# Performance work log

Measured on AMD Instinct MI355X. Metric: run time of the kernel, lower is better.

Reference implementation:

```python
import jax, jax.numpy as jnp
import numpy as np

B, T, I, H, C = 4096, 512, 3, 32, 3  # batch, seq_len, input, hidden, classes


def setup_inputs() -> dict:
    key = jax.random.key(0)
    ks = jax.random.split(key, 7)
    s = 1.0 / np.sqrt(H)  # PyTorch LSTM init scale
    return {
        "x": jax.random.normal(ks[0], (B, T, I), dtype=jnp.float32),
        "W_ih": jax.random.normal(ks[1], (4 * H, I), dtype=jnp.float32) * s,
        "W_hh": jax.random.normal(ks[2], (4 * H, H), dtype=jnp.float32) * s,
        "b_ih": jax.random.normal(ks[3], (4 * H,), dtype=jnp.float32) * s,
        "b_hh": jax.random.normal(ks[4], (4 * H,), dtype=jnp.float32) * s,
        "W_fc": jax.random.normal(ks[5], (C, H), dtype=jnp.float32) * s,
        "b_fc": jax.random.normal(ks[6], (C,), dtype=jnp.float32) * s,
    }


def reference(x, W_ih, W_hh, b_ih, b_hh, W_fc, b_fc):
    # Precompute input contribution to all gates for every timestep: (B,T,4H)
    xg = jnp.einsum("bti,gi->btg", x, W_ih) + b_ih + b_hh
    h0 = jnp.zeros((x.shape[0], H), dtype=x.dtype)
    c0 = jnp.zeros_like(h0)

    def step(carry, xt):
        h, c = carry
        g = xt + h @ W_hh.T  # (B,4H)
        i_g, f_g, g_g, o_g = jnp.split(g, 4, axis=-1)  # PyTorch gate order i,f,g,o
        i_g = jax.nn.sigmoid(i_g)
        f_g = jax.nn.sigmoid(f_g)
        g_g = jnp.tanh(g_g)
        o_g = jax.nn.sigmoid(o_g)
        c = f_g * c + i_g * g_g
        h = o_g * jnp.tanh(c)
        return (h, c), None

    (h_last, _), _ = jax.lax.scan(step, (h0, c0), jnp.swapaxes(xg, 0, 1))
    return h_last @ W_fc.T + b_fc  # (B, num_classes)
```

## Files before the change

kernel.cpp:

```cpp
#include <hip/hip_runtime.h>
#include <cstdint>

#define B_TOT 4096
#define T_LEN 512
#define CHUNK 128
#define LOG2E 1.44269504088896340736f
#define HSTR  40

typedef _Float16 f16x8 __attribute__((ext_vector_type(8)));
typedef _Float16 f16x4 __attribute__((ext_vector_type(4)));
typedef float    f32x4 __attribute__((ext_vector_type(4)));

__device__ __forceinline__ float ex2(float v)  { return __builtin_amdgcn_exp2f(v); }
__device__ __forceinline__ float rcp_(float v) { return __builtin_amdgcn_rcpf(v); }

__global__ __launch_bounds__(256, 2)
void lstm_b8p(const float* __restrict__ x,
              const float* __restrict__ W_ih,
              const float* __restrict__ W_hh,
              const float* __restrict__ b_ih,
              const float* __restrict__ b_hh,
              const float* __restrict__ W_fc,
              const float* __restrict__ b_fc,
              float* __restrict__ out)
{
    __shared__ __align__(16) _Float16 hbuf[2][8][HSTR];
    __shared__ __align__(16) _Float16 xbuf[CHUNK][8][4];

    const int tid  = threadIdx.x;
    const int wave = tid >> 6;
    const int lane = tid & 63;
    const int n    = lane & 15;
    const int kq   = lane >> 4;
    const int nb   = n & 7;
    const int tb   = blockIdx.x * 8;

    const int   gate_m = n & 3;
    const int   hl_m   = n >> 2;
    const int   R1     = gate_m * 32 + 8 * wave + hl_m;
    const int   R2     = R1 + 4;
    const float sm     = (gate_m == 2) ? (-2.0f * LOG2E) : (-LOG2E);

    f16x8 aW1, aW2;
#pragma unroll
    for (int j = 0; j < 8; ++j) {
        aW1[j] = (_Float16)(sm * W_hh[R1 * 32 + 8 * kq + j]);
        aW2[j] = (_Float16)(sm * W_hh[R2 * 32 + 8 * kq + j]);
    }
    f16x8 a21 = {}, a22 = {};
    if (kq == 0) {
        a21[0] = (_Float16)(sm * W_ih[R1 * 3 + 0]);
        a21[1] = (_Float16)(sm * W_ih[R1 * 3 + 1]);
        a21[2] = (_Float16)(sm * W_ih[R1 * 3 + 2]);
        a21[3] = (_Float16)(sm * (b_ih[R1] + b_hh[R1]));
        a22[0] = (_Float16)(sm * W_ih[R2 * 3 + 0]);
        a22[1] = (_Float16)(sm * W_ih[R2 * 3 + 1]);
        a22[2] = (_Float16)(sm * W_ih[R2 * 3 + 2]);
        a22[3] = (_Float16)(sm * (b_ih[R2] + b_hh[R2]));
    }

    const int hid_s = 8 * wave + kq + ((n >> 3) ? 4 : 0);

    if (tid < 160) ((int*)&hbuf[0][0][0])[tid] = 0;

    const float K2 = -2.0f * LOG2E;
    float c = 0.0f;
    const f32x4 z = {0.f, 0.f, 0.f, 0.f};
    f32x4 accx1, accx2;

    if (blockIdx.x & 256) __builtin_amdgcn_s_sleep(5);

    for (int tc = 0; tc < T_LEN; tc += CHUNK) {
#pragma unroll
        for (int s = 0; s < 4; ++s) {
            const int idx = tid + s * 256;
            const int tl = idx >> 3, m = idx & 7;
            const float* xp = x + ((size_t)(tb + m) * T_LEN + (tc + tl)) * 3;
            f16x4 v;
            v[0] = (_Float16)xp[0]; v[1] = (_Float16)xp[1];
            v[2] = (_Float16)xp[2]; v[3] = (_Float16)1.0f;
            *(f16x4*)&xbuf[tl][m][0] = v;
        }
        __syncthreads();

        {
            const f16x4 xv = *(const f16x4*)&xbuf[0][nb][0];
            const f16x8 b2 = __builtin_shufflevector(xv, xv, 0, 1, 2, 3, 0, 1, 2, 3);
            accx1 = __builtin_amdgcn_mfma_f32_16x16x32_f16(a21, b2, z, 0, 0, 0);
            accx2 = __builtin_amdgcn_mfma_f32_16x16x32_f16(a22, b2, z, 0, 0, 0);
        }

#pragma unroll 2
        for (int tt = 0; tt < CHUNK; ++tt) {
            const int p = tt & 1;

            const f16x8 bh  = *(const f16x8*)&hbuf[p][nb][8 * kq];
            const f32x4 ac1 = __builtin_amdgcn_mfma_f32_16x16x32_f16(aW1, bh, accx1, 0, 0, 0);
            const f32x4 ac2 = __builtin_amdgcn_mfma_f32_16x16x32_f16(aW2, bh, accx2, 0, 0, 0);

            const bool hi = (n >> 3) != 0;
            const float a0 = hi ? ac2[0] : ac1[0];
            const float a1 = hi ? ac2[1] : ac1[1];
            const float a2 = hi ? ac2[2] : ac1[2];
            const float a3 = hi ? ac2[3] : ac1[3];

            const float ei = ex2(a0), ef = ex2(a1), eg = ex2(a2), eo = ex2(a3);
            const float pi = 1.0f + ei, pf = 1.0f + ef, pg = 1.0f + eg;
            const float mg = 1.0f - eg;
            const float pp  = pi * pg;
            const float qn  = mg * pf;
            const float num = fmaf(c, pp, qn);
            c = num * rcp_(pf * pp);

            const float ec = ex2(c * K2);
            const float po = 1.0f + eo, pc = 1.0f + ec, mc = 1.0f - ec;
            const float h  = mc * rcp_(po * pc);

            hbuf[p ^ 1][nb][hid_s] = (_Float16)h;

            const int ttn = (tt + 1) & (CHUNK - 1);
            const f16x4 xv = *(const f16x4*)&xbuf[ttn][nb][0];
            const f16x8 b2 = __builtin_shufflevector(xv, xv, 0, 1, 2, 3, 0, 1, 2, 3);
            accx1 = __builtin_amdgcn_mfma_f32_16x16x32_f16(a21, b2, z, 0, 0, 0);
            accx2 = __builtin_amdgcn_mfma_f32_16x16x32_f16(a22, b2, z, 0, 0, 0);

            __syncthreads();
        }
    }

    if (tid < 24) {
        const int m = tid / 3, cc = tid % 3;
        float acc = b_fc[cc];
#pragma unroll
        for (int k = 0; k < 32; ++k)
            acc = fmaf(W_fc[cc * 32 + k], (float)hbuf[0][m][k], acc);
        out[(tb + m) * 3 + cc] = acc;
    }
}

extern "C" void kernel_launch(void* const* d_in, const int* in_sizes, int n_in,
                              void* d_out, int out_size, void* d_ws, size_t ws_size,
                              hipStream_t stream) {
    const float* x    = (const float*)d_in[0];
    const float* W_ih = (const float*)d_in[1];
    const float* W_hh = (const float*)d_in[2];
    const float* b_ih = (const float*)d_in[3];
    const float* b_hh = (const float*)d_in[4];
    const float* W_fc = (const float*)d_in[5];
    const float* b_fc = (const float*)d_in[6];
    float* out = (float*)d_out;

    dim3 grid(B_TOT / 8);
    dim3 block(256);
    lstm_b8p<<<grid, block, 0, stream>>>(x, W_ih, W_hh, b_ih, b_hh, W_fc, b_fc, out);
}
```

Baseline: 192.6 us.

## Process two 8-sequence tiles per block to interleave independent recurrences

Each block now handles 16 batch sequences as two independent 8-wide tiles, issuing four MFMAs per step and computing two gate/cell updates per thread. The grid is halved and launch bounds drop to one block per SM. The intent is to give each wave two independent dependency chains per timestep, so MFMA and transcendental latency can overlap and the per-step barrier cost is spread over more work. The staggered s_sleep for half the blocks is removed. In exchange there are fewer blocks (256) for the 256 CUs, higher register pressure, and longer serial work per step.

```diff
diff --git a/kernel.cpp b/kernel.cpp
--- a/kernel.cpp
+++ b/kernel.cpp
@@ -14,18 +14,18 @@
 __device__ __forceinline__ float ex2(float v)  { return __builtin_amdgcn_exp2f(v); }
 __device__ __forceinline__ float rcp_(float v) { return __builtin_amdgcn_rcpf(v); }
 
-__global__ __launch_bounds__(256, 2)
-void lstm_b8p(const float* __restrict__ x,
-              const float* __restrict__ W_ih,
-              const float* __restrict__ W_hh,
-              const float* __restrict__ b_ih,
-              const float* __restrict__ b_hh,
-              const float* __restrict__ W_fc,
-              const float* __restrict__ b_fc,
-              float* __restrict__ out)
+__global__ __launch_bounds__(256, 1)
+void lstm_dt(const float* __restrict__ x,
+             const float* __restrict__ W_ih,
+             const float* __restrict__ W_hh,
+             const float* __restrict__ b_ih,
+             const float* __restrict__ b_hh,
+             const float* __restrict__ W_fc,
+             const float* __restrict__ b_fc,
+             float* __restrict__ out)
 {
-    __shared__ __align__(16) _Float16 hbuf[2][8][HSTR];
-    __shared__ __align__(16) _Float16 xbuf[CHUNK][8][4];
+    __shared__ __align__(16) _Float16 hbuf[2][16][HSTR];
+    __shared__ __align__(16) _Float16 xbuf[CHUNK][16][4];
 
     const int tid  = threadIdx.x;
     const int wave = tid >> 6;
@@ -33,7 +33,7 @@
     const int n    = lane & 15;
     const int kq   = lane >> 4;
     const int nb   = n & 7;
-    const int tb   = blockIdx.x * 8;
+    const int tb   = blockIdx.x * 16;
 
     const int   gate_m = n & 3;
     const int   hl_m   = n >> 2;
@@ -61,20 +61,20 @@
 
     const int hid_s = 8 * wave + kq + ((n >> 3) ? 4 : 0);
 
-    if (tid < 160) ((int*)&hbuf[0][0][0])[tid] = 0;
+    for (int i = tid; i < 320; i += 256) ((int*)&hbuf[0][0][0])[i] = 0;
 
     const float K2 = -2.0f * LOG2E;
-    float c = 0.0f;
+    float cA = 0.0f, cB = 0.0f;
     const f32x4 z = {0.f, 0.f, 0.f, 0.f};
-    f32x4 accx1, accx2;
+    f32x4 ax1A, ax2A, ax1B, ax2B;
 
-    if (blockIdx.x & 256) __builtin_amdgcn_s_sleep(5);
+    const bool hi = (n >> 3) != 0;
 
     for (int tc = 0; tc < T_LEN; tc += CHUNK) {
 #pragma unroll
-        for (int s = 0; s < 4; ++s) {
+        for (int s = 0; s < 8; ++s) {
             const int idx = tid + s * 256;
-            const int tl = idx >> 3, m = idx & 7;
+            const int tl = idx >> 4, m = idx & 15;
             const float* xp = x + ((size_t)(tb + m) * T_LEN + (tc + tl)) * 3;
             f16x4 v;
             v[0] = (_Float16)xp[0]; v[1] = (_Float16)xp[1];
@@ -84,51 +84,76 @@
         __syncthreads();
 
         {
-            const f16x4 xv = *(const f16x4*)&xbuf[0][nb][0];
-            const f16x8 b2 = __builtin_shufflevector(xv, xv, 0, 1, 2, 3, 0, 1, 2, 3);
-            accx1 = __builtin_amdgcn_mfma_f32_16x16x32_f16(a21, b2, z, 0, 0, 0);
-            accx2 = __builtin_amdgcn_mfma_f32_16x16x32_f16(a22, b2, z, 0, 0, 0);
+            const f16x4 xa = *(const f16x4*)&xbuf[0][nb][0];
+            const f16x4 xb = *(const f16x4*)&xbuf[0][nb + 8][0];
+            const f16x8 bA = __builtin_shufflevector(xa, xa, 0, 1, 2, 3, 0, 1, 2, 3);
+            const f16x8 bB = __builtin_shufflevector(xb, xb, 0, 1, 2, 3, 0, 1, 2, 3);
+            ax1A = __builtin_amdgcn_mfma_f32_16x16x32_f16(a21, bA, z, 0, 0, 0);
+            ax2A = __builtin_amdgcn_mfma_f32_16x16x32_f16(a22, bA, z, 0, 0, 0);
+            ax1B = __builtin_amdgcn_mfma_f32_16x16x32_f16(a21, bB, z, 0, 0, 0);
+            ax2B = __builtin_amdgcn_mfma_f32_16x16x32_f16(a22, bB, z, 0, 0, 0);
         }
 
 #pragma unroll 2
         for (int tt = 0; tt < CHUNK; ++tt) {
             const int p = tt & 1;
 
-            const f16x8 bh  = *(const f16x8*)&hbuf[p][nb][8 * kq];
-            const f32x4 ac1 = __builtin_amdgcn_mfma_f32_16x16x32_f16(aW1, bh, accx1, 0, 0, 0);
-            const f32x4 ac2 = __builtin_amdgcn_mfma_f32_16x16x32_f16(aW2, bh, accx2, 0, 0, 0);
+            const f16x8 bhA = *(const f16x8*)&hbuf[p][nb][8 * kq];
+            const f16x8 bhB = *(const f16x8*)&hbuf[p][nb + 8][8 * kq];
 
-            const bool hi = (n >> 3) != 0;
-            const float a0 = hi ? ac2[0] : ac1[0];
-            const float a1 = hi ? ac2[1] : ac1[1];
-            const float a2 = hi ? ac2[2] : ac1[2];
-            const float a3 = hi ? ac2[3] : ac1[3];
+            const f32x4 acA1 = __builtin_amdgcn_mfma_f32_16x16x32_f16(aW1, bhA, ax1A, 0, 0, 0);
+            const f32x4 acA2 = __builtin_amdgcn_mfma_f32_16x16x32_f16(aW2, bhA, ax2A, 0, 0, 0);
+            const f32x4 acB1 = __builtin_amdgcn_mfma_f32_16x16x32_f16(aW1, bhB, ax1B, 0, 0, 0);
+            const f32x4 acB2 = __builtin_amdgcn_mfma_f32_16x16x32_f16(aW2, bhB, ax2B, 0, 0, 0);
 
-            const float ei = ex2(a0), ef = ex2(a1), eg = ex2(a2), eo = ex2(a3);
-            const float pi = 1.0f + ei, pf = 1.0f + ef, pg = 1.0f + eg;
-            const float mg = 1.0f - eg;
-            const float pp  = pi * pg;
-            const float qn  = mg * pf;
-            const float num = fmaf(c, pp, qn);
-            c = num * rcp_(pf * pp);
-
-            const float ec = ex2(c * K2);
-            const float po = 1.0f + eo, pc = 1.0f + ec, mc = 1.0f - ec;
-            const float h  = mc * rcp_(po * pc);
-
-            hbuf[p ^ 1][nb][hid_s] = (_Float16)h;
+            {
+                const float a0 = hi ? acA2[0] : acA1[0];
+                const float a1 = hi ? acA2[1] : acA1[1];
+                const float a2 = hi ? acA2[2] : acA1[2];
+                const float a3 = hi ? acA2[3] : acA1[3];
+                const float ei = ex2(a0), ef = ex2(a1), eg = ex2(a2), eo = ex2(a3);
+                const float pi = 1.0f + ei, pf = 1.0f + ef, pg = 1.0f + eg;
+                const float mg = 1.0f - eg;
+                const float pp = pi * pg, qn = mg * pf;
+                const float num = fmaf(cA, pp, qn);
+                cA = num * rcp_(pf * pp);
+                const float ec = ex2(cA * K2);
+                const float po = 1.0f + eo, pc = 1.0f + ec, mc = 1.0f - ec;
+                const float h = mc * rcp_(po * pc);
+                hbuf[p ^ 1][nb][hid_s] = (_Float16)h;
+            }
+            {
+                const float a0 = hi ? acB2[0] : acB1[0];
+                const float a1 = hi ? acB2[1] : acB1[1];
+                const float a2 = hi ? acB2[2] : acB1[2];
+                const float a3 = hi ? acB2[3] : acB1[3];
+                const float ei = ex2(a0), ef = ex2(a1), eg = ex2(a2), eo = ex2(a3);
+                const float pi = 1.0f + ei, pf = 1.0f + ef, pg = 1.0f + eg;
+                const float mg = 1.0f - eg;
+                const float pp = pi * pg, qn = mg * pf;
+                const float num = fmaf(cB, pp, qn);
+                cB = num * rcp_(pf * pp);
+                const float ec = ex2(cB * K2);
+                const float po = 1.0f + eo, pc = 1.0f + ec, mc = 1.0f - ec;
+                const float h = mc * rcp_(po * pc);
+                hbuf[p ^ 1][nb + 8][hid_s] = (_Float16)h;
+            }
 
             const int ttn = (tt + 1) & (CHUNK - 1);
-            const f16x4 xv = *(const f16x4*)&xbuf[ttn][nb][0];
-            const f16x8 b2 = __builtin_shufflevector(xv, xv, 0, 1, 2, 3, 0, 1, 2, 3);
-            accx1 = __builtin_amdgcn_mfma_f32_16x16x32_f16(a21, b2, z, 0, 0, 0);
-            accx2 = __builtin_amdgcn_mfma_f32_16x16x32_f16(a22, b2, z, 0, 0, 0);
+            const f16x4 xa = *(const f16x4*)&xbuf[ttn][nb][0];
+            const f16x4 xb = *(const f16x4*)&xbuf[ttn][nb + 8][0];
+            const f16x8 bA = __builtin_shufflevector(xa, xa, 0, 1, 2, 3, 0, 1, 2, 3);
+            const f16x8 bB = __builtin_shufflevector(xb, xb, 0, 1, 2, 3, 0, 1, 2, 3);
+            ax1A = __builtin_amdgcn_mfma_f32_16x16x32_f16(a21, bA, z, 0, 0, 0);
+            ax2A = __builtin_amdgcn_mfma_f32_16x16x32_f16(a22, bA, z, 0, 0, 0);
+            ax1B = __builtin_amdgcn_mfma_f32_16x16x32_f16(a21, bB, z, 0, 0, 0);
+            ax2B = __builtin_amdgcn_mfma_f32_16x16x32_f16(a22, bB, z, 0, 0, 0);
 
             __syncthreads();
         }
     }
 
-    if (tid < 24) {
+    if (tid < 48) {
         const int m = tid / 3, cc = tid % 3;
         float acc = b_fc[cc];
 #pragma unroll
@@ -150,7 +175,7 @@
     const float* b_fc = (const float*)d_in[6];
     float* out = (float*)d_out;
 
-    dim3 grid(B_TOT / 8);
+    dim3 grid(B_TOT / 16);
     dim3 block(256);
-    lstm_b8p<<<grid, block, 0, stream>>>(x, W_ih, W_hh, b_ih, b_hh, W_fc, b_fc, out);
+    lstm_dt<<<grid, block, 0, stream>>>(x, W_ih, W_hh, b_ih, b_hh, W_fc, b_fc, out);
 }
```

New measurement: 249.9 us. +29.7%, slower.
